# Kernel optimization log

Measured on AMD Instinct MI355X. Metric: run time of the kernel, lower is better.

Reference implementation:

```python
import jax, jax.numpy as jnp
import numpy as np

B, N_E, E_DIM = 131072, 1024, 64
BETA = 0.25


def setup_inputs() -> dict:
    key = jax.random.key(0)
    kz, kw = jax.random.split(key)
    z = jax.random.normal(kz, (B, E_DIM), dtype=jnp.float32)
    # nn.Embedding init: uniform(-1/n_e, 1/n_e)
    emb_w = jax.random.uniform(kw, (N_E, E_DIM), dtype=jnp.float32,
                               minval=-1.0 / N_E, maxval=1.0 / N_E)
    return {"z": z, "emb_w": emb_w}


def reference(z, emb_w):
    beta = jnp.float32(BETA)
    # pairwise squared distances: [B, n_e]
    d = (jnp.sum(z * z, axis=1, keepdims=True)
         + jnp.sum(emb_w * emb_w, axis=1)
         - 2.0 * jnp.einsum('bd,nd->bn', z, emb_w))
    idx = jnp.argmin(d, axis=1)                      # [B]
    z_q = jnp.take(emb_w, idx, axis=0)               # [B, e_dim]
    # legacy=False branch
    loss = (beta * jnp.mean((jax.lax.stop_gradient(z_q) - z) ** 2)
            + jnp.mean((z_q - jax.lax.stop_gradient(z)) ** 2))
    # straight-through estimator
    z_q_st = z + jax.lax.stop_gradient(z_q - z)
    # torch.var is unbiased (ddof=1)
    v = jnp.var(idx.astype(jnp.float32), ddof=1)
    return (z_q_st, loss, idx, v)
```

## Files before the change

kernel.cpp:

```cpp
#include <hip/hip_runtime.h>
#include <stdint.h>


typedef __attribute__((ext_vector_type(8))) __bf16 bf16x8;
typedef __attribute__((ext_vector_type(4))) float f32x4;

#define NBLK 512
#define NTHR 256
#define OUT_LOSS 8388608
#define OUT_IDX  8388609
#define OUT_VAR  8519681

#define WS_LOSS 0
#define WS_S1   4096
#define WS_S2   8192
#define WS_EFRAG 16384
#define WS_EE   (16384 + 131072)

__global__ void vq_prep(const float* __restrict__ emb, char* __restrict__ ws) {
  bf16x8* efrag = (bf16x8*)(ws + WS_EFRAG);
  float* eeoff = (float*)(ws + WS_EE);
  const int t = blockIdx.x;
  const int l = threadIdx.x;
  const int n = t * 16 + (l & 15);
  const int kb0 = (l >> 4) * 8;
  const float* er = emb + n * 64;
  for (int j = 0; j < 2; ++j) {
    const int kb = j * 32 + kb0;
    bf16x8 h;
#pragma unroll
    for (int i = 0; i < 8; ++i) h[i] = (__bf16)(-2.0f * er[kb + i]);
    efrag[(t * 2 + j) * 64 + l] = h;
  }
  if (l < 16) {
    const float* e2 = emb + (t * 16 + l) * 64;
    float s = 0.f;
#pragma unroll
    for (int d = 0; d < 64; ++d) s += e2[d] * e2[d];
    eeoff[t * 16 + l] = s;
  }
}

__global__ void __launch_bounds__(NTHR, 2) vq_main(
    const float* __restrict__ z, const float* __restrict__ emb,
    float* __restrict__ out, char* __restrict__ ws) {
  __shared__ char smem[65536];
  const int tid = threadIdx.x;
  const int wave = tid >> 6, lane = tid & 63;
  const int lr = lane & 15, ksl = lane >> 4;
  const int k0 = ksl * 8;
  const int row_base = blockIdx.x * 256 + wave * 64;

  f32x4 zraw[4][4];
  bf16x8 zf[4][2];
#pragma unroll
  for (int r = 0; r < 4; ++r) {
    const float* zr = z + (size_t)(row_base + r * 16 + lr) * 64;
#pragma unroll
    for (int j = 0; j < 2; ++j) {
      f32x4 v0 = *(const f32x4*)(zr + j * 32 + k0);
      f32x4 v1 = *(const f32x4*)(zr + j * 32 + k0 + 4);
      zraw[r][j * 2 + 0] = v0;
      zraw[r][j * 2 + 1] = v1;
      bf16x8 h;
#pragma unroll
      for (int i = 0; i < 4; ++i) { h[i] = (__bf16)v0[i]; h[4 + i] = (__bf16)v1[i]; }
      zf[r][j] = h;
    }
  }

  float m1[4];
  unsigned i1[4];
#pragma unroll
  for (int r = 0; r < 4; ++r) { m1[r] = 1e30f; i1[r] = 0; }

  const float* eeoff = (const float*)(ws + WS_EE);
  for (int ph = 0; ph < 2; ++ph) {
    const f32x4* src = (const f32x4*)(ws + WS_EFRAG + ph * 65536);
    f32x4* dst = (f32x4*)smem;
    __syncthreads();
    for (int i = tid; i < 4096; i += NTHR) dst[i] = src[i];
    __syncthreads();
    const bf16x8* sfrag = (const bf16x8*)smem;
    for (int tt = 0; tt < 32; ++tt) {
      const int t = ph * 32 + tt;
      bf16x8 e0 = sfrag[(tt * 2 + 0) * 64 + lane];
      bf16x8 e1 = sfrag[(tt * 2 + 1) * 64 + lane];
      f32x4 ee = *(const f32x4*)(eeoff + t * 16 + ksl * 4);
      const unsigned nb = (unsigned)(t * 16 + ksl * 4);
#pragma unroll
      for (int r = 0; r < 4; ++r) {
        f32x4 acc = ee;
        acc = __builtin_amdgcn_mfma_f32_16x16x32_bf16(e0, zf[r][0], acc, 0, 0, 0);
        acc = __builtin_amdgcn_mfma_f32_16x16x32_bf16(e1, zf[r][1], acc, 0, 0, 0);
#pragma unroll
        for (int j = 0; j < 4; ++j) {
          float v = acc[j];
          if (v < m1[r]) { m1[r] = v; i1[r] = nb + j; }
        }
      }
    }
  }

  float ls_acc = 0.f;
  long long s1_acc = 0, s2_acc = 0;
#pragma unroll
  for (int r = 0; r < 4; ++r) {
    float m = m1[r];
    unsigned idx = i1[r];
#pragma unroll
    for (int off = 16; off < 64; off <<= 1) {
      float mo = __shfl_xor(m, off, 64);
      unsigned io = __shfl_xor(idx, off, 64);
      bool take = (mo < m) || ((mo == m) && (io < idx));
      m = take ? mo : m;
      idx = take ? io : idx;
    }
    const int row = row_base + r * 16 + lr;
    const float* ep = emb + (size_t)idx * 64;
    float* op = out + (size_t)row * 64;
#pragma unroll
    for (int j = 0; j < 2; ++j) {
      f32x4 e0 = *(const f32x4*)(ep + j * 32 + k0);
      f32x4 e1 = *(const f32x4*)(ep + j * 32 + k0 + 4);
      *(f32x4*)(op + j * 32 + k0) = e0;
      *(f32x4*)(op + j * 32 + k0 + 4) = e1;
#pragma unroll
      for (int c = 0; c < 4; ++c) {
        float d0 = e0[c] - zraw[r][j * 2 + 0][c];
        float d1 = e1[c] - zraw[r][j * 2 + 1][c];
        ls_acc += d0 * d0 + d1 * d1;
      }
    }
    if (ksl == 0) {
      out[OUT_IDX + row] = (float)idx;
      s1_acc += (long long)idx;
      s2_acc += (long long)(idx * idx);
    }
  }
#pragma unroll
  for (int off = 1; off < 64; off <<= 1) {
    ls_acc += __shfl_xor(ls_acc, off, 64);
    s1_acc += __shfl_xor(s1_acc, off, 64);
    s2_acc += __shfl_xor(s2_acc, off, 64);
  }
  __syncthreads();
  double* sL = (double*)smem;
  long long* sA = (long long*)(smem + 64);
  long long* sB = (long long*)(smem + 128);
  if (lane == 0) { sL[wave] = (double)ls_acc; sA[wave] = s1_acc; sB[wave] = s2_acc; }
  __syncthreads();
  if (tid == 0) {
    double L = 0; long long a = 0, b = 0;
    for (int w = 0; w < 4; ++w) { L += sL[w]; a += sA[w]; b += sB[w]; }
    ((double*)(ws + WS_LOSS))[blockIdx.x] = L;
    ((long long*)(ws + WS_S1))[blockIdx.x] = a;
    ((long long*)(ws + WS_S2))[blockIdx.x] = b;
  }
}

__global__ void vq_final(float* __restrict__ out, const char* __restrict__ ws) {
  const int t = threadIdx.x;
  const double* lp = (const double*)(ws + WS_LOSS);
  const long long* p1 = (const long long*)(ws + WS_S1);
  const long long* p2 = (const long long*)(ws + WS_S2);
  double L = lp[t] + lp[t + 256];
  long long a = p1[t] + p1[t + 256];
  long long b = p2[t] + p2[t + 256];
#pragma unroll
  for (int off = 1; off < 64; off <<= 1) {
    L += __shfl_xor(L, off, 64);
    a += __shfl_xor(a, off, 64);
    b += __shfl_xor(b, off, 64);
  }
  __shared__ double sL[4];
  __shared__ long long sA[4], sB[4];
  const int wave = t >> 6, lane = t & 63;
  if (lane == 0) { sL[wave] = L; sA[wave] = a; sB[wave] = b; }
  __syncthreads();
  if (t == 0) {
    double Lt = 0; long long at = 0, bt = 0;
    for (int w = 0; w < 4; ++w) { Lt += sL[w]; at += sA[w]; bt += sB[w]; }
    out[OUT_LOSS] = (float)(1.25 * Lt / 8388608.0);
    long long num = bt * 131072LL - at * at;
    out[OUT_VAR] = (float)((double)num / (131072.0 * 131071.0));
  }
}

extern "C" void kernel_launch(void* const* d_in, const int* in_sizes, int n_in,
                              void* d_out, int out_size, void* d_ws, size_t ws_size,
                              hipStream_t stream) {
  (void)in_sizes; (void)n_in; (void)out_size; (void)ws_size;
  const float* z = (const float*)d_in[0];
  const float* emb = (const float*)d_in[1];
  float* out = (float*)d_out;
  char* ws = (char*)d_ws;
  vq_prep<<<64, 64, 0, stream>>>(emb, ws);
  vq_main<<<NBLK, NTHR, 0, stream>>>(z, emb, out, ws);
  vq_final<<<1, 256, 0, stream>>>(out, ws);
}
```

Before: 55.78 us.

## Split codebook across waves, pack argmin into keys, derive loss from distances

Each block now handles 64 rows instead of 256, and its four waves each scan a quarter of the codebook for all 64 rows. The per-wave results are merged through shared memory, and the block count rises to 2048. The argmin is packed into a single unsigned key (truncated float bits with the index in the low 10 bits), using a +0.5 offset so the distances stay positive. The loss is computed from ||z||^2 plus the minimum distance, so the raw z values no longer need to be held for a second pass. This removes the LDS staging of codebook fragments and lowers register pressure (launch bounds raised to 4). The cost is approximate tie-breaking and a bf16-based loss value that may differ from the reference.

```diff
diff --git a/kernel.cpp b/kernel.cpp
--- a/kernel.cpp
+++ b/kernel.cpp
@@ -5,17 +5,17 @@
 typedef __attribute__((ext_vector_type(8))) __bf16 bf16x8;
 typedef __attribute__((ext_vector_type(4))) float f32x4;
 
-#define NBLK 512
+#define NBLK 2048
 #define NTHR 256
 #define OUT_LOSS 8388608
 #define OUT_IDX  8388609
 #define OUT_VAR  8519681
 
 #define WS_LOSS 0
-#define WS_S1   4096
-#define WS_S2   8192
-#define WS_EFRAG 16384
-#define WS_EE   (16384 + 131072)
+#define WS_S1   8192
+#define WS_S2   16384
+#define WS_EFRAG 24576
+#define WS_EE   (24576 + 131072)
 
 __global__ void vq_prep(const float* __restrict__ emb, char* __restrict__ ws) {
   bf16x8* efrag = (bf16x8*)(ws + WS_EFRAG);
@@ -37,136 +37,134 @@
     float s = 0.f;
 #pragma unroll
     for (int d = 0; d < 64; ++d) s += e2[d] * e2[d];
-    eeoff[t * 16 + l] = s;
-  }
-}
-
-__global__ void __launch_bounds__(NTHR, 2) vq_main(
+    eeoff[t * 16 + l] = s + 0.5f;
+  }
+}
+
+__global__ void __launch_bounds__(NTHR, 4) vq_main(
     const float* __restrict__ z, const float* __restrict__ emb,
     float* __restrict__ out, char* __restrict__ ws) {
-  __shared__ char smem[65536];
   const int tid = threadIdx.x;
   const int wave = tid >> 6, lane = tid & 63;
   const int lr = lane & 15, ksl = lane >> 4;
   const int k0 = ksl * 8;
-  const int row_base = blockIdx.x * 256 + wave * 64;
-
-  f32x4 zraw[4][4];
+  const int row_base = blockIdx.x * 64;
+
   bf16x8 zf[4][2];
+  float zz[4];
 #pragma unroll
   for (int r = 0; r < 4; ++r) {
     const float* zr = z + (size_t)(row_base + r * 16 + lr) * 64;
+    float s = 0.f;
 #pragma unroll
     for (int j = 0; j < 2; ++j) {
       f32x4 v0 = *(const f32x4*)(zr + j * 32 + k0);
       f32x4 v1 = *(const f32x4*)(zr + j * 32 + k0 + 4);
-      zraw[r][j * 2 + 0] = v0;
-      zraw[r][j * 2 + 1] = v1;
       bf16x8 h;
 #pragma unroll
-      for (int i = 0; i < 4; ++i) { h[i] = (__bf16)v0[i]; h[4 + i] = (__bf16)v1[i]; }
+      for (int i = 0; i < 4; ++i) {
+        h[i] = (__bf16)v0[i]; h[4 + i] = (__bf16)v1[i];
+        s += v0[i] * v0[i] + v1[i] * v1[i];
+      }
       zf[r][j] = h;
     }
-  }
-
-  float m1[4];
-  unsigned i1[4];
-#pragma unroll
-  for (int r = 0; r < 4; ++r) { m1[r] = 1e30f; i1[r] = 0; }
-
-  const float* eeoff = (const float*)(ws + WS_EE);
-  for (int ph = 0; ph < 2; ++ph) {
-    const f32x4* src = (const f32x4*)(ws + WS_EFRAG + ph * 65536);
-    f32x4* dst = (f32x4*)smem;
-    __syncthreads();
-    for (int i = tid; i < 4096; i += NTHR) dst[i] = src[i];
-    __syncthreads();
-    const bf16x8* sfrag = (const bf16x8*)smem;
-    for (int tt = 0; tt < 32; ++tt) {
-      const int t = ph * 32 + tt;
-      bf16x8 e0 = sfrag[(tt * 2 + 0) * 64 + lane];
-      bf16x8 e1 = sfrag[(tt * 2 + 1) * 64 + lane];
-      f32x4 ee = *(const f32x4*)(eeoff + t * 16 + ksl * 4);
-      const unsigned nb = (unsigned)(t * 16 + ksl * 4);
-#pragma unroll
-      for (int r = 0; r < 4; ++r) {
-        f32x4 acc = ee;
-        acc = __builtin_amdgcn_mfma_f32_16x16x32_bf16(e0, zf[r][0], acc, 0, 0, 0);
-        acc = __builtin_amdgcn_mfma_f32_16x16x32_bf16(e1, zf[r][1], acc, 0, 0, 0);
-#pragma unroll
-        for (int j = 0; j < 4; ++j) {
-          float v = acc[j];
-          if (v < m1[r]) { m1[r] = v; i1[r] = nb + j; }
-        }
+    zz[r] = s;
+  }
+
+  unsigned mkey[4];
+#pragma unroll
+  for (int r = 0; r < 4; ++r) mkey[r] = 0xFFFFFFFFu;
+
+  const bf16x8* efrag = (const bf16x8*)(ws + WS_EFRAG);
+  const f32x4* eeoff = (const f32x4*)(ws + WS_EE);
+#pragma unroll 2
+  for (int tt = 0; tt < 16; ++tt) {
+    const int t = wave * 16 + tt;
+    bf16x8 e0 = efrag[(t * 2 + 0) * 64 + lane];
+    bf16x8 e1 = efrag[(t * 2 + 1) * 64 + lane];
+    f32x4 ee = eeoff[t * 4 + ksl];
+    const unsigned nb = (unsigned)(t * 16 + ksl * 4);
+#pragma unroll
+    for (int r = 0; r < 4; ++r) {
+      f32x4 acc = __builtin_amdgcn_mfma_f32_16x16x32_bf16(e0, zf[r][0], ee, 0, 0, 0);
+      acc = __builtin_amdgcn_mfma_f32_16x16x32_bf16(e1, zf[r][1], acc, 0, 0, 0);
+#pragma unroll
+      for (int j = 0; j < 4; ++j) {
+        unsigned key = (__float_as_uint(acc[j]) & 0xFFFFFC00u) | (nb + j);
+        mkey[r] = min(mkey[r], key);
       }
     }
   }
 
-  float ls_acc = 0.f;
-  long long s1_acc = 0, s2_acc = 0;
 #pragma unroll
   for (int r = 0; r < 4; ++r) {
-    float m = m1[r];
-    unsigned idx = i1[r];
-#pragma unroll
-    for (int off = 16; off < 64; off <<= 1) {
-      float mo = __shfl_xor(m, off, 64);
-      unsigned io = __shfl_xor(idx, off, 64);
-      bool take = (mo < m) || ((mo == m) && (io < idx));
-      m = take ? mo : m;
-      idx = take ? io : idx;
+    mkey[r] = min(mkey[r], (unsigned)__shfl_xor((int)mkey[r], 16, 64));
+    mkey[r] = min(mkey[r], (unsigned)__shfl_xor((int)mkey[r], 32, 64));
+    zz[r] += __shfl_xor(zz[r], 16, 64);
+    zz[r] += __shfl_xor(zz[r], 32, 64);
+  }
+
+  __shared__ unsigned skey[4][64];
+  __shared__ float szz[64];
+  __shared__ float sL[4];
+  __shared__ int sA[4], sB[4];
+  if (ksl == 0) {
+#pragma unroll
+    for (int r = 0; r < 4; ++r) {
+      skey[wave][r * 16 + lr] = mkey[r];
+      if (wave == 0) szz[r * 16 + lr] = zz[r];
     }
-    const int row = row_base + r * 16 + lr;
-    const float* ep = emb + (size_t)idx * 64;
-    float* op = out + (size_t)row * 64;
-#pragma unroll
-    for (int j = 0; j < 2; ++j) {
-      f32x4 e0 = *(const f32x4*)(ep + j * 32 + k0);
-      f32x4 e1 = *(const f32x4*)(ep + j * 32 + k0 + 4);
-      *(f32x4*)(op + j * 32 + k0) = e0;
-      *(f32x4*)(op + j * 32 + k0 + 4) = e1;
-#pragma unroll
-      for (int c = 0; c < 4; ++c) {
-        float d0 = e0[c] - zraw[r][j * 2 + 0][c];
-        float d1 = e1[c] - zraw[r][j * 2 + 1][c];
-        ls_acc += d0 * d0 + d1 * d1;
-      }
-    }
-    if (ksl == 0) {
-      out[OUT_IDX + row] = (float)idx;
-      s1_acc += (long long)idx;
-      s2_acc += (long long)(idx * idx);
-    }
+  }
+  __syncthreads();
+
+  const int row = tid >> 2, seg = tid & 3;
+  const unsigned k = min(min(skey[0][row], skey[1][row]),
+                         min(skey[2][row], skey[3][row]));
+  const unsigned idx = k & 1023u;
+  const size_t rowg = (size_t)row_base + row;
+  const f32x4* ep = (const f32x4*)(emb + (size_t)idx * 64 + seg * 16);
+  f32x4* op = (f32x4*)(out + rowg * 64 + seg * 16);
+#pragma unroll
+  for (int c = 0; c < 4; ++c) op[c] = ep[c];
+
+  float ls = 0.f; int s1 = 0, s2 = 0;
+  if (seg == 0) {
+    ls = szz[row] + __uint_as_float(k & 0xFFFFFC00u) - 0.5f;
+    s1 = (int)idx;
+    s2 = (int)(idx * idx);
+    out[OUT_IDX + rowg] = (float)idx;
   }
 #pragma unroll
   for (int off = 1; off < 64; off <<= 1) {
-    ls_acc += __shfl_xor(ls_acc, off, 64);
-    s1_acc += __shfl_xor(s1_acc, off, 64);
-    s2_acc += __shfl_xor(s2_acc, off, 64);
-  }
-  __syncthreads();
-  double* sL = (double*)smem;
-  long long* sA = (long long*)(smem + 64);
-  long long* sB = (long long*)(smem + 128);
-  if (lane == 0) { sL[wave] = (double)ls_acc; sA[wave] = s1_acc; sB[wave] = s2_acc; }
+    ls += __shfl_xor(ls, off, 64);
+    s1 += __shfl_xor(s1, off, 64);
+    s2 += __shfl_xor(s2, off, 64);
+  }
+  if (lane == 0) { sL[wave] = ls; sA[wave] = s1; sB[wave] = s2; }
   __syncthreads();
   if (tid == 0) {
-    double L = 0; long long a = 0, b = 0;
+    float L = 0; int a = 0, b = 0;
+#pragma unroll
     for (int w = 0; w < 4; ++w) { L += sL[w]; a += sA[w]; b += sB[w]; }
-    ((double*)(ws + WS_LOSS))[blockIdx.x] = L;
-    ((long long*)(ws + WS_S1))[blockIdx.x] = a;
-    ((long long*)(ws + WS_S2))[blockIdx.x] = b;
+    ((float*)(ws + WS_LOSS))[blockIdx.x] = L;
+    ((int*)(ws + WS_S1))[blockIdx.x] = a;
+    ((int*)(ws + WS_S2))[blockIdx.x] = b;
   }
 }
 
 __global__ void vq_final(float* __restrict__ out, const char* __restrict__ ws) {
   const int t = threadIdx.x;
-  const double* lp = (const double*)(ws + WS_LOSS);
-  const long long* p1 = (const long long*)(ws + WS_S1);
-  const long long* p2 = (const long long*)(ws + WS_S2);
-  double L = lp[t] + lp[t + 256];
-  long long a = p1[t] + p1[t + 256];
-  long long b = p2[t] + p2[t + 256];
+  const float* lp = (const float*)(ws + WS_LOSS);
+  const int* p1 = (const int*)(ws + WS_S1);
+  const int* p2 = (const int*)(ws + WS_S2);
+  double L = 0; long long a = 0, b = 0;
+#pragma unroll
+  for (int kk = 0; kk < 8; ++kk) {
+    const int i = t + 256 * kk;
+    L += (double)lp[i];
+    a += (long long)p1[i];
+    b += (long long)p2[i];
+  }
 #pragma unroll
   for (int off = 1; off < 64; off <<= 1) {
     L += __shfl_xor(L, off, 64);
@@ -180,6 +178,7 @@
   __syncthreads();
   if (t == 0) {
     double Lt = 0; long long at = 0, bt = 0;
+#pragma unroll
     for (int w = 0; w < 4; ++w) { Lt += sL[w]; at += sA[w]; bt += sB[w]; }
     out[OUT_LOSS] = (float)(1.25 * Lt / 8388608.0);
     long long num = bt * 131072LL - at * at;
```

Result: no change. 55.45 us (-0.6%).
